# Kernel optimization log

Measured on AMD Instinct MI355X. Metric: run time of the kernel, lower is better.

Reference implementation:

```python
import jax, jax.numpy as jnp
import numpy as np

N = 20000
E = 640000
R = 8          # num_rels == num_bases (basis regularizer with num_bases=-1)
B = 8
IN_SIZE = 128
HID = 256      # 4 * fea_dimen
FEA = 64
TIME = 2880
POI = 12


def setup_inputs() -> dict:
    key = jax.random.key(0)
    ks = jax.random.split(key, 20)
    s = 0.02
    inp = {
        'src': jax.random.randint(ks[0], (E,), 0, N),
        'dst': jax.random.randint(ks[1], (E,), 0, N),
        'etype': jax.random.randint(ks[2], (E,), 0, R),
        'poi_distribution': jax.random.normal(ks[3], (N, POI), jnp.float32),
        'time_distribution': jax.random.normal(ks[4], (N, TIME), jnp.float32),
        'road_feature': jax.random.normal(ks[5], (N, IN_SIZE), jnp.float32),
        # input projections
        'poi_w': jax.random.normal(ks[6], (POI, FEA), jnp.float32) * s,
        'poi_b': jnp.zeros((FEA,), jnp.float32),
        'time_w': jax.random.normal(ks[7], (TIME, 2 * FEA), jnp.float32) * s,
        'time_b': jnp.zeros((2 * FEA,), jnp.float32),
        'road_w': jax.random.normal(ks[8], (IN_SIZE, FEA), jnp.float32) * s,
        'road_b': jnp.zeros((FEA,), jnp.float32),
        # RelGraphConv layer 1 (basis decomposition)
        'basis1': jax.random.normal(ks[9], (B, HID, HID), jnp.float32) * s,
        'coef1': jax.random.normal(ks[10], (R, B), jnp.float32) * s,
        'loop_w1': jax.random.normal(ks[11], (HID, HID), jnp.float32) * s,
        'bias1': jnp.zeros((HID,), jnp.float32),
        # RelGraphConv layer 2
        'basis2': jax.random.normal(ks[12], (B, HID, HID), jnp.float32) * s,
        'coef2': jax.random.normal(ks[13], (R, B), jnp.float32) * s,
        'loop_w2': jax.random.normal(ks[14], (HID, HID), jnp.float32) * s,
        'bias2': jnp.zeros((HID,), jnp.float32),
    }
    return inp


def _rel_graph_conv(h, src, dst, etype, basis, coef, loop_w, bias):
    # W_r = sum_b coef[r,b] * basis[b]  -> (R, HID, HID), small
    W = jnp.einsum('rb,bio->rio', coef, basis)
    # transform every node by every relation weight, then gather per edge
    y = jnp.einsum('ni,rio->nro', h, W)          # (N, R, HID)
    msgs = y[src, etype]                          # (E, HID) gather
    agg = jax.ops.segment_sum(msgs, dst, num_segments=h.shape[0])  # scatter-sum
    return agg + h @ loop_w + bias


def reference(src, dst, etype, poi_distribution, time_distribution, road_feature,
              poi_w, poi_b, time_w, time_b, road_w, road_b,
              basis1, coef1, loop_w1, bias1, basis2, coef2, loop_w2, bias2):
    poi_feat = poi_distribution @ poi_w + poi_b       # (N, 64)
    time_feat = time_distribution @ time_w + time_b   # (N, 128)
    road_feat = road_feature @ road_w + road_b        # (N, 64)
    feat = jnp.concatenate([poi_feat, time_feat, road_feat], axis=1)  # (N, 256)
    h = _rel_graph_conv(feat, src, dst, etype, basis1, coef1, loop_w1, bias1)
    h = jax.nn.relu(h)  # dropout=0.0 -> identity
    h = _rel_graph_conv(h, src, dst, etype, basis2, coef2, loop_w2, bias2)
    return h
```

## Files before the change

kernel.cpp:

```cpp
#include <hip/hip_runtime.h>

#define NN 20000
#define NE 640000
#define NR 8
#define NB 8
#define HID 256
#define KPOI 12
#define KTIME 2880
#define KROAD 128
#define NK (NN * NR)
#define NS 9
#define KCAT (NS * HID)

typedef __attribute__((ext_vector_type(8))) short bf8_t;
typedef __attribute__((ext_vector_type(4))) float f4_t;

__device__ inline unsigned short f2bf(float f) {
  unsigned int u = __float_as_uint(f);
  u += 0x7FFF + ((u >> 16) & 1);
  return (unsigned short)(u >> 16);
}
__device__ inline float bf2f(unsigned short h) {
  return __uint_as_float((unsigned int)h << 16);
}

__device__ inline void gl_lds16(const void* g, void* l) {
  __builtin_amdgcn_global_load_lds(
      (const __attribute__((address_space(1))) void*)g,
      (__attribute__((address_space(3))) void*)l, 16, 0, 0);
}

__global__ __launch_bounds__(256) void hist_k(const int* __restrict__ dst,
                                              const int* __restrict__ et,
                                              int* __restrict__ counts) {
  int e = blockIdx.x * 256 + threadIdx.x;
  if (e < NE) atomicAdd(&counts[dst[e] * NR + et[e]], 1);
}

__global__ __launch_bounds__(256) void scan_all(
    const int* __restrict__ counts, int* __restrict__ offs,
    int* __restrict__ cursor, int* __restrict__ bsums,
    int* __restrict__ counter) {
  __shared__ int sh[256];
  __shared__ int base_sh;
  const int bid = blockIdx.x;
  const int t = threadIdx.x;
  const int gbase = bid * 1024;
  int v[4], run[4];
  int s = 0;
#pragma unroll
  for (int j = 0; j < 4; ++j) {
    int idx = gbase + t * 4 + j;
    v[j] = (idx < NK) ? counts[idx] : 0;
    s += v[j];
  }
  sh[t] = s;
  __syncthreads();
  for (int off = 1; off < 256; off <<= 1) {
    int x = (t >= off) ? sh[t - off] : 0;
    __syncthreads();
    sh[t] += x;
    __syncthreads();
  }
  {
    int r = sh[t] - s;
#pragma unroll
    for (int j = 0; j < 4; ++j) { run[j] = r; r += v[j]; }
  }
  if (t == 255) {
    bsums[bid] = sh[255];
    __threadfence();
    atomicAdd(counter, 1);
  }
  if (t == 0) {
    while (atomicAdd(counter, 0) < (int)gridDim.x) {}
    __threadfence();
    int b = 0;
    for (int j = 0; j < bid; ++j) b += atomicAdd(&bsums[j], 0);
    base_sh = b;
  }
  __syncthreads();
  const int base = base_sh;
#pragma unroll
  for (int j = 0; j < 4; ++j) {
    int idx = gbase + t * 4 + j;
    if (idx < NK) {
      int val = run[j] + base;
      offs[idx] = val;
      cursor[idx] = val;
    }
  }
  if (bid == 0 && t == 0) offs[NK] = NE;
}

__global__ __launch_bounds__(256) void fill_k(const int* __restrict__ src,
                                              const int* __restrict__ dst,
                                              const int* __restrict__ et,
                                              int* __restrict__ cursor,
                                              unsigned short* __restrict__ ssrc) {
  int e = blockIdx.x * 256 + threadIdx.x;
  if (e < NE) {
    int key = dst[e] * NR + et[e];
    int p = atomicAdd(&cursor[key], 1);
    ssrc[p] = (unsigned short)src[e];
  }
}

#define BK 16
__device__ inline void sgemm_body(
    int M, int Nn, int K,
    const float* __restrict__ A, int lda,
    const float* __restrict__ B, int ldb,
    const float* __restrict__ bias,
    unsigned short* __restrict__ C, int ldc, int brow, char* lds)
{
  constexpr int BM = 64, BN = 64, TM = 4, TN = 4;
  constexpr int SA = BM + 4;
  constexpr int SB = BN + 4;
  float* As = (float*)lds;
  float* Bs = (float*)(lds + 4352);
  const int tid = threadIdx.x;
  constexpr int TCOLS = BN / TN;
  const int row0 = (tid / TCOLS) * TM;
  const int col0 = (tid % TCOLS) * TN;

  float acc[TM][TN] = {};

  for (int kb = 0; kb < K; kb += BK) {
    {
      int i = tid;
      int r = i >> 2, q = (i & 3) * 4;
      int grow = brow + r, gk = kb + q;
      if (grow < M && gk + 3 < K) {
        float4 v = *(const float4*)(A + (size_t)grow * lda + gk);
        As[(q + 0) * SA + r] = v.x;
        As[(q + 1) * SA + r] = v.y;
        As[(q + 2) * SA + r] = v.z;
        As[(q + 3) * SA + r] = v.w;
      } else {
#pragma unroll
        for (int j = 0; j < 4; ++j)
          As[(q + j) * SA + r] =
              (grow < M && gk + j < K) ? A[(size_t)grow * lda + gk + j] : 0.f;
      }
    }
    {
      int i = tid;
      int k = i / (BN / 4), cq = (i % (BN / 4)) * 4;
      int gk = kb + k;
      float4 v = {0.f, 0.f, 0.f, 0.f};
      if (gk < K) {
        if (cq + 3 < Nn) {
          v = *(const float4*)(B + (size_t)gk * ldb + cq);
        } else {
#pragma unroll
          for (int j = 0; j < 4; ++j)
            if (cq + j < Nn) (&v.x)[j] = B[(size_t)gk * ldb + cq + j];
        }
      }
      *(float4*)(&Bs[k * SB + cq]) = v;
    }
    __syncthreads();
#pragma unroll
    for (int kk = 0; kk < BK; ++kk) {
      float a[TM], bb[TN];
      *(float4*)(&a[0]) = *(const float4*)(&As[kk * SA + row0]);
      *(float4*)(&bb[0]) = *(const float4*)(&Bs[kk * SB + col0]);
#pragma unroll
      for (int i = 0; i < TM; ++i)
#pragma unroll
        for (int j = 0; j < TN; ++j)
          acc[i][j] += a[i] * bb[j];
    }
    __syncthreads();
  }

  float bcache[TN];
#pragma unroll
  for (int j = 0; j < TN; ++j) bcache[j] = bias[col0 + j];
#pragma unroll
  for (int i = 0; i < TM; ++i) {
    int row = brow + row0 + i;
    if (row >= M) continue;
#pragma unroll
    for (int j = 0; j < TN; ++j)
      C[(size_t)row * ldc + col0 + j] = f2bf(acc[i][j] + bcache[j]);
  }
}

__global__ __launch_bounds__(256) void prep_proj_k(
    const float* __restrict__ loop_w1, const float* __restrict__ loop_w2,
    const float* __restrict__ time_w,
    const float* __restrict__ coef1, const float* __restrict__ basis1,
    const float* __restrict__ coef2, const float* __restrict__ basis2,
    const float* __restrict__ poi_dist, const float* __restrict__ poi_w,
    const float* __restrict__ poi_b,
    const float* __restrict__ road_feat, const float* __restrict__ road_w,
    const float* __restrict__ road_b,
    unsigned short* __restrict__ Wc1, unsigned short* __restrict__ Wc2,
    unsigned short* __restrict__ TWT, unsigned short* __restrict__ hbuf)
{
  __shared__ __align__(16) char lds[8704];
  const int b = blockIdx.x;
  const int to = threadIdx.x & 63;
  const int tq = threadIdx.x >> 6;

  if (b < 378) {
    unsigned short (*T)[66] = (unsigned short (*)[66])lds;
    if (b < 256) {
      const int lr = b >> 4;
      const int tile = b & 15;
      const int i0 = ((tile >> 2) & 3) * 64, o0 = (tile & 3) * 64;
      const float* coef  = (lr < NR) ? coef1 : coef2;
      const float* basis = (lr < NR) ? basis1 : basis2;
      unsigned short* Wc = (lr < NR) ? Wc1 : Wc2;
      const int r = lr & 7;
      float cf[NB];
#pragma unroll
      for (int q = 0; q < NB; ++q) cf[q] = coef[r * NB + q];
#pragma unroll
      for (int k = 0; k < 16; ++k) {
        int i_loc = tq * 16 + k;
        int i = i0 + i_loc;
        float acc = 0.f;
#pragma unroll
        for (int q = 0; q < NB; ++q)
          acc += cf[q] * basis[((size_t)(q * HID + i)) * HID + o0 + to];
        T[i_loc][to] = f2bf(acc);
      }
      __syncthreads();
#pragma unroll
      for (int k = 0; k < 16; ++k) {
        int o_loc = tq * 16 + k;
        Wc[(size_t)(o0 + o_loc) * KCAT + r * HID + i0 + to] = T[to][o_loc];
      }
    } else if (b < 288) {
      const int j = b - 256;
      const int layer = j >> 4;
      const int tile = j & 15;
      const int i0 = ((tile >> 2) & 3) * 64, o0 = (tile & 3) * 64;
      const float* lw = layer ? loop_w2 : loop_w1;
      unsigned short* Wc = layer ? Wc2 : Wc1;
#pragma unroll
      for (int k = 0; k < 16; ++k) {
        int i_loc = tq * 16 + k;
        T[i_loc][to] = f2bf(lw[(size_t)(i0 + i_loc) * HID + o0 + to]);
      }
      __syncthreads();
#pragma unroll
      for (int k = 0; k < 16; ++k) {
        int o_loc = tq * 16 + k;
        Wc[(size_t)(o0 + o_loc) * KCAT + NR * HID + i0 + to] = T[to][o_loc];
      }
    } else {
      const int j = b - 288;
      const int r0 = (j >> 1) * 64, c0 = (j & 1) * 64;
#pragma unroll
      for (int k = 0; k < 16; ++k) {
        int r_loc = tq * 16 + k;
        T[r_loc][to] = f2bf(time_w[(size_t)(r0 + r_loc) * 128 + c0 + to]);
      }
      __syncthreads();
#pragma unroll
      for (int k = 0; k < 16; ++k) {
        int c_loc = tq * 16 + k;
        TWT[(size_t)(c0 + c_loc) * KTIME + r0 + to] = T[to][c_loc];
      }
    }
  } else if (b < 691) {
    sgemm_body(NN, 64, KPOI, poi_dist, KPOI, poi_w, 64, poi_b,
               hbuf + 0, HID, (b - 378) * 64, lds);
  } else {
    sgemm_body(NN, 64, KROAD, road_feat, KROAD, road_w, 64, road_b,
               hbuf + 192, HID, (b - 691) * 64, lds);
  }
}

__global__ __launch_bounds__(512) void mfma_time2(
    const float* __restrict__ A,
    const unsigned short* __restrict__ BT,
    const float* __restrict__ bias,
    unsigned short* __restrict__ featb)
{
  __shared__ __align__(16) char ldsA[2 * 32 * 128];
  __shared__ __align__(16) char ldsB[2 * 128 * 128];
  const int tid = threadIdx.x;
  const int lane = tid & 63;
  const int w = tid >> 6;
  const int g = w >> 2;
  const int cb = w & 3;
  const int brow = blockIdx.x * 32;
  const int c8sw = (lane & 7) ^ (lane >> 3);

  f4_t acc[2][2];
#pragma unroll
  for (int i = 0; i < 2; ++i)
#pragma unroll
    for (int j = 0; j < 2; ++j) acc[i][j] = (f4_t){0.f, 0.f, 0.f, 0.f};

  for (int i = 0; i < 23; ++i) {
    {
      int sg = tid >> 8, r = (tid >> 3) & 31, c8 = tid & 7;
      int step = sg * 23 + i;
      unsigned short hh[8] = {0, 0, 0, 0, 0, 0, 0, 0};
      if (step < 45) {
        const float* ap = A + (size_t)(brow + r) * KTIME + step * 64 + c8 * 8;
        f4_t v0 = *(const f4_t*)ap;
        f4_t v1 = *(const f4_t*)(ap + 4);
#pragma unroll
        for (int j = 0; j < 4; ++j) { hh[j] = f2bf(v0[j]); hh[4 + j] = f2bf(v1[j]); }
      }
      *(bf8_t*)(ldsA + sg * 4096 + r * 128 + ((c8 * 16) ^ ((r & 7) << 4))) =
          *(bf8_t*)hh;
    }
#pragma unroll
    for (int it = 0; it < 4; ++it) {
      int s0 = (w << 6) + it * 512;
      int sg = s0 >> 10;
      int r0 = (s0 >> 3) & 127;
      int step = sg * 23 + i;
      if (step < 45) {
        int r = r0 + (lane >> 3);
        gl_lds16(BT + (size_t)r * KTIME + step * 64 + c8sw * 8,
                 ldsB + sg * 16384 + r0 * 128);
      }
    }
    __syncthreads();
    if (g * 23 + i < 45) {
#pragma unroll
      for (int ks = 0; ks < 2; ++ks) {
        const int kbyte = ks * 64 + (lane >> 4) * 16;
        bf8_t af[2], bfr[2];
#pragma unroll
        for (int mi = 0; mi < 2; ++mi) {
          int m = mi * 16 + (lane & 15);
          af[mi] = *(const bf8_t*)(
              ldsA + g * 4096 + m * 128 + (kbyte ^ ((m & 7) << 4)));
        }
#pragma unroll
        for (int ni = 0; ni < 2; ++ni) {
          int n = cb * 32 + ni * 16 + (lane & 15);
          bfr[ni] = *(const bf8_t*)(
              ldsB + g * 16384 + n * 128 + (kbyte ^ ((n & 7) << 4)));
        }
#pragma unroll
        for (int mi = 0; mi < 2; ++mi)
#pragma unroll
          for (int ni = 0; ni < 2; ++ni)
            acc[mi][ni] = __builtin_amdgcn_mfma_f32_16x16x32_bf16(
                af[mi], bfr[ni], acc[mi][ni], 0, 0, 0);
      }
    }
    __syncthreads();
  }

  float* rb = (float*)ldsB;
  if (g == 1) {
#pragma unroll
    for (int mi = 0; mi < 2; ++mi)
#pragma unroll
      for (int ni = 0; ni < 2; ++ni)
#pragma unroll
        for (int j = 0; j < 4; ++j)
          rb[(cb * 64 + lane) * 16 + (mi * 2 + ni) * 4 + j] = acc[mi][ni][j];
  }
  __syncthreads();
  if (g == 0) {
    const int rq = (lane >> 4) * 4;
    const int cl = lane & 15;
#pragma unroll
    for (int ni = 0; ni < 2; ++ni) {
      int c = cb * 32 + ni * 16 + cl;
      float bv = bias[c];
#pragma unroll
      for (int mi = 0; mi < 2; ++mi) {
#pragma unroll
        for (int j = 0; j < 4; ++j) {
          float v = acc[mi][ni][j] +
                    rb[(cb * 64 + lane) * 16 + (mi * 2 + ni) * 4 + j] + bv;
          int row = brow + mi * 16 + rq + j;
          featb[(size_t)row * 256 + 64 + c] = f2bf(v);
        }
      }
    }
  }
}

__global__ __launch_bounds__(256) void agg_k(
    const int* __restrict__ offs, const unsigned short* __restrict__ ssrc,
    const unsigned short* __restrict__ hin, unsigned short* __restrict__ Zc) {
  int d = (blockIdx.x * 256 + threadIdx.x) >> 6;
  int lane = threadIdx.x & 63;
  if (d >= NN) return;
  unsigned short* zrow = Zc + (size_t)d * KCAT;
  *(ushort4*)(zrow + NR * HID + lane * 4) =
      *(const ushort4*)(hin + (size_t)d * HID + lane * 4);
  int ob[NR + 1];
#pragma unroll
  for (int r = 0; r <= NR; ++r) ob[r] = offs[d * NR + r];
#pragma unroll 1
  for (int q = 0; q < NR; ++q) {
    int e = ob[q], hi = ob[q + 1];
    f4_t az = {0.f, 0.f, 0.f, 0.f};
    for (; e + 4 <= hi; e += 4) {
      int s0 = ssrc[e], s1 = ssrc[e + 1], s2 = ssrc[e + 2], s3 = ssrc[e + 3];
      ushort4 u0 = *(const ushort4*)(hin + (size_t)s0 * HID + lane * 4);
      ushort4 u1 = *(const ushort4*)(hin + (size_t)s1 * HID + lane * 4);
      ushort4 u2 = *(const ushort4*)(hin + (size_t)s2 * HID + lane * 4);
      ushort4 u3 = *(const ushort4*)(hin + (size_t)s3 * HID + lane * 4);
      az.x += (bf2f(u0.x) + bf2f(u1.x)) + (bf2f(u2.x) + bf2f(u3.x));
      az.y += (bf2f(u0.y) + bf2f(u1.y)) + (bf2f(u2.y) + bf2f(u3.y));
      az.z += (bf2f(u0.z) + bf2f(u1.z)) + (bf2f(u2.z) + bf2f(u3.z));
      az.w += (bf2f(u0.w) + bf2f(u1.w)) + (bf2f(u2.w) + bf2f(u3.w));
    }
    for (; e < hi; ++e) {
      int s = ssrc[e];
      ushort4 u = *(const ushort4*)(hin + (size_t)s * HID + lane * 4);
      az.x += bf2f(u.x); az.y += bf2f(u.y);
      az.z += bf2f(u.z); az.w += bf2f(u.w);
    }
    unsigned short hz[4] = {f2bf(az.x), f2bf(az.y), f2bf(az.z), f2bf(az.w)};
    *(ushort4*)(zrow + q * HID + lane * 4) = *(ushort4*)hz;
  }
}

template<int EPI>
__global__ __launch_bounds__(512) void gemm_cat(
    const unsigned short* __restrict__ Zc,
    const unsigned short* __restrict__ Wc,
    const float* __restrict__ bias,
    float* __restrict__ C, unsigned short* __restrict__ hb)
{
  __shared__ __align__(16) char At[64 * 128];
  __shared__ __align__(16) char Bt[256 * 128];
  const int tid = threadIdx.x;
  const int lane = tid & 63;
  const int w = tid >> 6;
  const int wm = w >> 2;
  const int wn = w & 3;
  const int brow = blockIdx.x * 64;
  const bool full = (brow + 64 <= NN);
  const int c8sw = (lane & 7) ^ (lane >> 3);

  f4_t acc[2][4];
#pragma unroll
  for (int i = 0; i < 2; ++i)
#pragma unroll
    for (int j = 0; j < 4; ++j) acc[i][j] = (f4_t){0.f, 0.f, 0.f, 0.f};

  for (int kb = 0; kb < KCAT; kb += 64) {
    if (full) {
      int row = (w << 3) + (lane >> 3);
      gl_lds16(Zc + (size_t)(brow + row) * KCAT + kb + c8sw * 8,
               At + (w << 10));
    } else {
      int r = tid >> 3, c8 = tid & 7;
      int grow = brow + r;
      bf8_t v = {0, 0, 0, 0, 0, 0, 0, 0};
      if (grow < NN) v = *(const bf8_t*)(Zc + (size_t)grow * KCAT + kb + c8 * 8);
      *(bf8_t*)(At + r * 128 + ((c8 * 16) ^ ((r & 7) << 4))) = v;
    }
#pragma unroll
    for (int it = 0; it < 4; ++it) {
      int n0 = (w << 3) + it * 64;
      int n = n0 + (lane >> 3);
      gl_lds16(Wc + (size_t)n * KCAT + kb + c8sw * 8, Bt + n0 * 128);
    }
    __syncthreads();
#pragma unroll
    for (int ks = 0; ks < 2; ++ks) {
      const int kbyte = ks * 64 + (lane >> 4) * 16;
      bf8_t af[2], bfr[4];
#pragma unroll
      for (int mi = 0; mi < 2; ++mi) {
        int m = wm * 32 + mi * 16 + (lane & 15);
        af[mi] = *(const bf8_t*)(At + m * 128 + (kbyte ^ ((m & 7) << 4)));
      }
#pragma unroll
      for (int ni = 0; ni < 4; ++ni) {
        int n = wn * 64 + ni * 16 + (lane & 15);
        bfr[ni] = *(const bf8_t*)(Bt + n * 128 + (kbyte ^ ((n & 7) << 4)));
      }
#pragma unroll
      for (int mi = 0; mi < 2; ++mi)
#pragma unroll
        for (int ni = 0; ni < 4; ++ni)
          acc[mi][ni] = __builtin_amdgcn_mfma_f32_16x16x32_bf16(
              af[mi], bfr[ni], acc[mi][ni], 0, 0, 0);
    }
    __syncthreads();
  }

  const int rq = (lane >> 4) * 4;
  const int cl = lane & 15;
#pragma unroll
  for (int ni = 0; ni < 4; ++ni) {
    int c = wn * 64 + ni * 16 + cl;
    float bv = bias[c];
#pragma unroll
    for (int mi = 0; mi < 2; ++mi) {
#pragma unroll
      for (int j = 0; j < 4; ++j) {
        int row = brow + wm * 32 + mi * 16 + rq + j;
        if (row < NN) {
          size_t o = (size_t)row * HID + c;
          float v = acc[mi][ni][j] + bv;
          if (EPI == 0) C[o] = v;
          else          hb[o] = f2bf(fmaxf(v, 0.f));
        }
      }
    }
  }
}

extern "C" void kernel_launch(void* const* d_in, const int* in_sizes, int n_in,
                              void* d_out, int out_size, void* d_ws, size_t ws_size,
                              hipStream_t stream) {
  const int*   srcp      = (const int*)d_in[0];
  const int*   dstp      = (const int*)d_in[1];
  const int*   etypep    = (const int*)d_in[2];
  const float* poi_dist  = (const float*)d_in[3];
  const float* time_dist = (const float*)d_in[4];
  const float* road_feat = (const float*)d_in[5];
  const float* poi_w     = (const float*)d_in[6];
  const float* poi_b     = (const float*)d_in[7];
  const float* time_w    = (const float*)d_in[8];
  const float* time_b    = (const float*)d_in[9];
  const float* road_w    = (const float*)d_in[10];
  const float* road_b    = (const float*)d_in[11];
  const float* basis1    = (const float*)d_in[12];
  const float* coef1     = (const float*)d_in[13];
  const float* loop_w1   = (const float*)d_in[14];
  const float* bias1     = (const float*)d_in[15];
  const float* basis2    = (const float*)d_in[16];
  const float* coef2     = (const float*)d_in[17];
  const float* loop_w2   = (const float*)d_in[18];
  const float* bias2     = (const float*)d_in[19];

  float* out = (float*)d_out;

  char* ws = (char*)d_ws;
  unsigned short* Wc1    = (unsigned short*)(ws);
  unsigned short* Wc2    = (unsigned short*)(ws + 1179648);
  unsigned short* TWT    = (unsigned short*)(ws + 2359296);
  unsigned short* hbuf   = (unsigned short*)(ws + 3096576);
  unsigned short* Zcat   = (unsigned short*)(ws + 13336576);
  int*            offs   = (int*)  (ws + 105496576);
  int*            bsums  = (int*)  (ws + 106136592);
  unsigned short* ssrc   = (unsigned short*)(ws + 106137616);
  int*            cursor = (int*)  (ws + 107417616);
  int*            counts = (int*)Zcat;
  int*            counter = counts + NK;

  dim3 blk(256);

  hipMemsetAsync(counts, 0, (NK + 1) * sizeof(int), stream);
  hist_k<<<NE / 256, blk, 0, stream>>>(dstp, etypep, counts);
  scan_all<<<(NK + 1023) / 1024, blk, 0, stream>>>(counts, offs, cursor,
                                                   bsums, counter);
  fill_k<<<NE / 256, blk, 0, stream>>>(srcp, dstp, etypep, cursor, ssrc);

  prep_proj_k<<<1004, blk, 0, stream>>>(loop_w1, loop_w2, time_w,
                                        coef1, basis1, coef2, basis2,
                                        poi_dist, poi_w, poi_b,
                                        road_feat, road_w, road_b,
                                        Wc1, Wc2, TWT, hbuf);

  mfma_time2<<<NN / 32, 512, 0, stream>>>(time_dist, TWT, time_b, hbuf);

  agg_k<<<NN * 64 / 256, blk, 0, stream>>>(offs, ssrc, hbuf, Zcat);
  gemm_cat<1><<<(NN + 63) / 64, 512, 0, stream>>>(Zcat, Wc1, bias1, nullptr, hbuf);

  agg_k<<<NN * 64 / 256, blk, 0, stream>>>(offs, ssrc, hbuf, Zcat);
  gemm_cat<0><<<(NN + 63) / 64, 512, 0, stream>>>(Zcat, Wc2, bias2, out, nullptr);
}
```

Measured before the change: 399.0 us.

## Fuse graph CSR build kernels into projection and time-GEMM launches

The edge histogram is merged into the weight-prep/projection kernel and the CSR fill into the time-distribution MFMA kernel, with extra leading blocks handling edge work. The scan kernel's serial per-block prefix over block sums is replaced by a parallel in-block scan. The goal is fewer kernel launches and letting the independent graph preprocessing overlap with dense compute, at the cost of mixed-role blocks sharing the larger launch's resources such as the 512-thread block size and the enlarged LDS allocation.

```diff
diff --git a/kernel.cpp b/kernel.cpp
--- a/kernel.cpp
+++ b/kernel.cpp
@@ -28,82 +28,6 @@
   __builtin_amdgcn_global_load_lds(
       (const __attribute__((address_space(1))) void*)g,
       (__attribute__((address_space(3))) void*)l, 16, 0, 0);
-}
-
-__global__ __launch_bounds__(256) void hist_k(const int* __restrict__ dst,
-                                              const int* __restrict__ et,
-                                              int* __restrict__ counts) {
-  int e = blockIdx.x * 256 + threadIdx.x;
-  if (e < NE) atomicAdd(&counts[dst[e] * NR + et[e]], 1);
-}
-
-__global__ __launch_bounds__(256) void scan_all(
-    const int* __restrict__ counts, int* __restrict__ offs,
-    int* __restrict__ cursor, int* __restrict__ bsums,
-    int* __restrict__ counter) {
-  __shared__ int sh[256];
-  __shared__ int base_sh;
-  const int bid = blockIdx.x;
-  const int t = threadIdx.x;
-  const int gbase = bid * 1024;
-  int v[4], run[4];
-  int s = 0;
-#pragma unroll
-  for (int j = 0; j < 4; ++j) {
-    int idx = gbase + t * 4 + j;
-    v[j] = (idx < NK) ? counts[idx] : 0;
-    s += v[j];
-  }
-  sh[t] = s;
-  __syncthreads();
-  for (int off = 1; off < 256; off <<= 1) {
-    int x = (t >= off) ? sh[t - off] : 0;
-    __syncthreads();
-    sh[t] += x;
-    __syncthreads();
-  }
-  {
-    int r = sh[t] - s;
-#pragma unroll
-    for (int j = 0; j < 4; ++j) { run[j] = r; r += v[j]; }
-  }
-  if (t == 255) {
-    bsums[bid] = sh[255];
-    __threadfence();
-    atomicAdd(counter, 1);
-  }
-  if (t == 0) {
-    while (atomicAdd(counter, 0) < (int)gridDim.x) {}
-    __threadfence();
-    int b = 0;
-    for (int j = 0; j < bid; ++j) b += atomicAdd(&bsums[j], 0);
-    base_sh = b;
-  }
-  __syncthreads();
-  const int base = base_sh;
-#pragma unroll
-  for (int j = 0; j < 4; ++j) {
-    int idx = gbase + t * 4 + j;
-    if (idx < NK) {
-      int val = run[j] + base;
-      offs[idx] = val;
-      cursor[idx] = val;
-    }
-  }
-  if (bid == 0 && t == 0) offs[NK] = NE;
-}
-
-__global__ __launch_bounds__(256) void fill_k(const int* __restrict__ src,
-                                              const int* __restrict__ dst,
-                                              const int* __restrict__ et,
-                                              int* __restrict__ cursor,
-                                              unsigned short* __restrict__ ssrc) {
-  int e = blockIdx.x * 256 + threadIdx.x;
-  if (e < NE) {
-    int key = dst[e] * NR + et[e];
-    int p = atomicAdd(&cursor[key], 1);
-    ssrc[p] = (unsigned short)src[e];
-  }
 }
 
 #define BK 16
@@ -188,7 +112,9 @@
   }
 }
 
-__global__ __launch_bounds__(256) void prep_proj_k(
+__global__ __launch_bounds__(256) void hist_prep_k(
+    const int* __restrict__ dstp, const int* __restrict__ etp,
+    int* __restrict__ counts,
     const float* __restrict__ loop_w1, const float* __restrict__ loop_w2,
     const float* __restrict__ time_w,
     const float* __restrict__ coef1, const float* __restrict__ basis1,
@@ -201,7 +127,13 @@
     unsigned short* __restrict__ TWT, unsigned short* __restrict__ hbuf)
 {
   __shared__ __align__(16) char lds[8704];
-  const int b = blockIdx.x;
+  int b = blockIdx.x;
+  if (b < 2500) {
+    int e = b * 256 + threadIdx.x;
+    atomicAdd(&counts[dstp[e] * NR + etp[e]], 1);
+    return;
+  }
+  b -= 2500;
   const int to = threadIdx.x & 63;
   const int tq = threadIdx.x >> 6;
 
@@ -276,20 +208,96 @@
   }
 }
 
-__global__ __launch_bounds__(512) void mfma_time2(
+__global__ __launch_bounds__(256) void scan_all(
+    const int* __restrict__ counts, int* __restrict__ offs,
+    int* __restrict__ cursor, int* __restrict__ bsums,
+    int* __restrict__ counter) {
+  __shared__ int sh[256];
+  const int bid = blockIdx.x;
+  const int t = threadIdx.x;
+  const int nblk = gridDim.x;
+  const int gbase = bid * 1024;
+  int v[4], run[4];
+  int s = 0;
+#pragma unroll
+  for (int j = 0; j < 4; ++j) {
+    int idx = gbase + t * 4 + j;
+    v[j] = (idx < NK) ? counts[idx] : 0;
+    s += v[j];
+  }
+  sh[t] = s;
+  __syncthreads();
+  for (int off = 1; off < 256; off <<= 1) {
+    int x = (t >= off) ? sh[t - off] : 0;
+    __syncthreads();
+    sh[t] += x;
+    __syncthreads();
+  }
+  {
+    int r = sh[t] - s;
+#pragma unroll
+    for (int j = 0; j < 4; ++j) { run[j] = r; r += v[j]; }
+  }
+  if (t == 255) {
+    bsums[bid] = sh[255];
+    __threadfence();
+    atomicAdd(counter, 1);
+  }
+  if (t == 0) {
+    while (atomicAdd(counter, 0) < nblk) {}
+    __threadfence();
+  }
+  __syncthreads();
+  int bs = (t < nblk) ? atomicAdd(&bsums[t], 0) : 0;
+  __syncthreads();
+  sh[t] = bs;
+  __syncthreads();
+  for (int off = 1; off < 256; off <<= 1) {
+    int x = (t >= off) ? sh[t - off] : 0;
+    __syncthreads();
+    sh[t] += x;
+    __syncthreads();
+  }
+  const int base = (bid > 0) ? sh[bid - 1] : 0;
+#pragma unroll
+  for (int j = 0; j < 4; ++j) {
+    int idx = gbase + t * 4 + j;
+    if (idx < NK) {
+      int val = run[j] + base;
+      offs[idx] = val;
+      cursor[idx] = val;
+    }
+  }
+  if (bid == 0 && t == 0) offs[NK] = NE;
+}
+
+__global__ __launch_bounds__(512) void fill_time_k(
+    const int* __restrict__ srcp, const int* __restrict__ dstp,
+    const int* __restrict__ etp, int* __restrict__ cursor,
+    unsigned short* __restrict__ ssrc,
     const float* __restrict__ A,
     const unsigned short* __restrict__ BT,
     const float* __restrict__ bias,
     unsigned short* __restrict__ featb)
 {
-  __shared__ __align__(16) char ldsA[2 * 32 * 128];
-  __shared__ __align__(16) char ldsB[2 * 128 * 128];
+  __shared__ __align__(16) char lds[40960];
+  int b = blockIdx.x;
+  if (b < 1250) {
+    int e = b * 512 + threadIdx.x;
+    int key = dstp[e] * NR + etp[e];
+    int p = atomicAdd(&cursor[key], 1);
+    ssrc[p] = (unsigned short)srcp[e];
+    return;
+  }
+  b -= 1250;
+  char* ldsA = lds;
+  char* ldsB = lds + 8192;
   const int tid = threadIdx.x;
   const int lane = tid & 63;
   const int w = tid >> 6;
   const int g = w >> 2;
   const int cb = w & 3;
-  const int brow = blockIdx.x * 32;
+  const int brow = b * 32;
   const int c8sw = (lane & 7) ^ (lane >> 3);
 
   f4_t acc[2][2];
@@ -555,18 +563,19 @@
   dim3 blk(256);
 
   hipMemsetAsync(counts, 0, (NK + 1) * sizeof(int), stream);
-  hist_k<<<NE / 256, blk, 0, stream>>>(dstp, etypep, counts);
-  scan_all<<<(NK + 1023) / 1024, blk, 0, stream>>>(counts, offs, cursor,
-                                                   bsums, counter);
-  fill_k<<<NE / 256, blk, 0, stream>>>(srcp, dstp, etypep, cursor, ssrc);
-
-  prep_proj_k<<<1004, blk, 0, stream>>>(loop_w1, loop_w2, time_w,
+
+  hist_prep_k<<<3504, blk, 0, stream>>>(dstp, etypep, counts,
+                                        loop_w1, loop_w2, time_w,
                                         coef1, basis1, coef2, basis2,
                                         poi_dist, poi_w, poi_b,
                                         road_feat, road_w, road_b,
                                         Wc1, Wc2, TWT, hbuf);
 
-  mfma_time2<<<NN / 32, 512, 0, stream>>>(time_dist, TWT, time_b, hbuf);
+  scan_all<<<(NK + 1023) / 1024, blk, 0, stream>>>(counts, offs, cursor,
+                                                   bsums, counter);
+
+  fill_time_k<<<1875, 512, 0, stream>>>(srcp, dstp, etypep, cursor, ssrc,
+                                        time_dist, TWT, time_b, hbuf);
 
   agg_k<<<NN * 64 / 256, blk, 0, stream>>>(offs, ssrc, hbuf, Zcat);
   gemm_cat<1><<<(NN + 63) / 64, 512, 0, stream>>>(Zcat, Wc1, bias1, nullptr, hbuf);
```

Result: faster. 379.8 us (-4.8%).
